# Performance work log

Hardware: AMD Instinct MI355X
Metric: run time of the kernel (lower is better)

## Reference

```python
import jax, jax.numpy as jnp
import numpy as np

B, L, D = 16384, 50, 32  # batch, history length, embedding_dim
NU, NI, NC = 100000, 100000, 1000


def setup_inputs() -> dict:
    key = jax.random.key(0)
    ks = jax.random.split(key, 16)
    customer_id = jax.random.randint(ks[0], (B,), 0, NU)
    candidate_good = jax.random.randint(ks[1], (B,), 0, NI)
    candidate_class = jax.random.randint(ks[2], (B,), 0, NC)
    history_goods = jax.random.randint(ks[3], (B, L), 0, NI)
    history_classes = jax.random.randint(ks[4], (B, L), 0, NC)
    user_table = jax.random.normal(ks[5], (NU, D), jnp.float32) * 0.05
    item_table = jax.random.normal(ks[6], (NI, D), jnp.float32) * 0.05
    item_table = item_table.at[0].set(0.0)  # padding_idx=0
    cat_table = jax.random.normal(ks[7], (NC, D), jnp.float32) * 0.05
    cat_table = cat_table.at[0].set(0.0)  # padding_idx=0
    # attention net: Linear(4*2D=256 -> 80), Linear(80 -> 1)
    aw1 = jax.random.normal(ks[8], (4 * 2 * D, 80), jnp.float32) * 0.05
    ab1 = jnp.zeros((80,), jnp.float32)
    aw2 = jax.random.normal(ks[9], (80, 1), jnp.float32) * 0.05
    ab2 = jnp.zeros((1,), jnp.float32)
    # final mlp: 5D=160 -> 256 -> 128 -> 1
    mw1 = jax.random.normal(ks[10], (5 * D, 256), jnp.float32) * 0.05
    mb1 = jnp.zeros((256,), jnp.float32)
    mw2 = jax.random.normal(ks[11], (256, 128), jnp.float32) * 0.05
    mb2 = jnp.zeros((128,), jnp.float32)
    mw3 = jax.random.normal(ks[12], (128, 1), jnp.float32) * 0.05
    mb3 = jnp.zeros((1,), jnp.float32)
    return dict(customer_id=customer_id, candidate_good=candidate_good,
                candidate_class=candidate_class, history_goods=history_goods,
                history_classes=history_classes, user_table=user_table,
                item_table=item_table, cat_table=cat_table,
                aw1=aw1, ab1=ab1, aw2=aw2, ab2=ab2,
                mw1=mw1, mb1=mb1, mw2=mw2, mb2=mb2, mw3=mw3, mb3=mb3)


def reference(customer_id, candidate_good, candidate_class, history_goods,
              history_classes, user_table, item_table, cat_table,
              aw1, ab1, aw2, ab2, mw1, mb1, mw2, mb2, mw3, mb3):
    user_emb = user_table[customer_id]                               # [B, D]
    cand = jnp.concatenate([item_table[candidate_good],
                            cat_table[candidate_class]], axis=-1)    # [B, 2D]
    hist = jnp.concatenate([item_table[history_goods],
                            cat_table[history_classes]], axis=-1)    # [B, L, 2D]
    q = jnp.broadcast_to(cand[:, None, :], hist.shape)               # [B, L, 2D]
    info = jnp.concatenate([q, hist, q - hist, q * hist], axis=-1)   # [B, L, 8D]
    h = jax.nn.relu(info @ aw1 + ab1)                                # [B, L, 80]
    scores = (h @ aw2 + ab2)[..., 0]                                 # [B, L]
    mask = history_goods != 0
    scores = jnp.where(mask, scores, -1e9)
    weights = jax.nn.softmax(scores, axis=1)                         # [B, L]
    att = jnp.einsum('bl,bld->bd', weights, hist)                    # [B, 2D]
    combined = jnp.concatenate([user_emb, cand, att], axis=-1)       # [B, 5D]
    z = jax.nn.relu(combined @ mw1 + mb1)
    z = jax.nn.relu(z @ mw2 + mb2)
    out = (z @ mw3 + mb3)[..., 0]                                    # [B]
    return out
```

## Files before the change

### kernel.cpp

```cpp
#include <hip/hip_runtime.h>
#include <hip/hip_bf16.h>
#include <math.h>

#define LHIST 50

typedef __attribute__((ext_vector_type(8))) short bf16x8;
typedef __attribute__((ext_vector_type(8))) unsigned short u16x8;
typedef __attribute__((ext_vector_type(4))) unsigned u32x4;
typedef __attribute__((ext_vector_type(4))) float f32x4;

__device__ __forceinline__ unsigned short f2bf(float f) {
    union { float f; unsigned u; } v; v.f = f;
    unsigned r = v.u + 0x7fff + ((v.u >> 16) & 1);
    return (unsigned short)(r >> 16);
}
__device__ __forceinline__ float bf2f(unsigned short h) {
    return __builtin_bit_cast(float, (unsigned)h << 16);
}
__device__ __forceinline__ unsigned pk2(float lo, float hi) {
    __hip_bfloat162 h = __float22bfloat162_rn(make_float2(lo, hi));
    unsigned u;
    __builtin_memcpy(&u, &h, 4);
    return u;
}
__device__ __forceinline__ f32x4 mfma16(bf16x8 a, bf16x8 b, f32x4 c) {
    return __builtin_amdgcn_mfma_f32_16x16x32_bf16(a, b, c, 0, 0, 0);
}
__device__ __forceinline__ bf16x8 mulq(u16x8 h, float4 qa, float4 qb) {
    u32x4 r;
    r[0] = pk2(bf2f(h[0]) * qa.x, bf2f(h[1]) * qa.y);
    r[1] = pk2(bf2f(h[2]) * qa.z, bf2f(h[3]) * qa.w);
    r[2] = pk2(bf2f(h[4]) * qb.x, bf2f(h[5]) * qb.y);
    r[3] = pk2(bf2f(h[6]) * qb.z, bf2f(h[7]) * qb.w);
    return __builtin_bit_cast(bf16x8, r);
}


__global__ void prep_kernel(const float* __restrict__ aw1,
                            const float* __restrict__ mw1,
                            const float* __restrict__ mw2,
                            const float* __restrict__ item_table,
                            const float* __restrict__ cat_table,
                            int itemN, int catN,
                            unsigned short* __restrict__ W13fb,
                            unsigned short* __restrict__ Bmfb,
                            unsigned short* __restrict__ W4fb,
                            unsigned short* __restrict__ W1f,
                            unsigned short* __restrict__ W2f,
                            unsigned short* __restrict__ itemb,
                            unsigned short* __restrict__ catb) {
    int i = blockIdx.x * 256 + threadIdx.x;
    int i8 = i * 8;
    if (i8 + 7 < itemN) {
        float4 a = *(const float4*)&item_table[i8];
        float4 b = *(const float4*)&item_table[i8 + 4];
        uint4 r;
        r.x = pk2(a.x, a.y); r.y = pk2(a.z, a.w);
        r.z = pk2(b.x, b.y); r.w = pk2(b.z, b.w);
        *(uint4*)&itemb[i8] = r;
    }
    if (i8 + 7 < catN) {
        float4 a = *(const float4*)&cat_table[i8];
        float4 b = *(const float4*)&cat_table[i8 + 4];
        uint4 r;
        r.x = pk2(a.x, a.y); r.y = pk2(a.z, a.w);
        r.z = pk2(b.x, b.y); r.w = pk2(b.z, b.w);
        *(uint4*)&catb[i8] = r;
    }
    if (i < 5120) {
        int kk = i / 80, n = i - kk * 80;
        int nt = n >> 4, colw = n & 15, ks = kk >> 5, r = kk & 31, qd = r >> 3, off = r & 7;
        int d = ((nt * 2 + ks) * 64 + qd * 16 + colw) * 8 + off;
        Bmfb[d]  = f2bf(aw1[(64 + kk) * 80 + n] - aw1[(128 + kk) * 80 + n]);
        W4fb[d]  = f2bf(aw1[(192 + kk) * 80 + n]);
        W13fb[d] = f2bf(aw1[kk * 80 + n] + aw1[(128 + kk) * 80 + n]);
    }
    if (i < 40960) {
        int kk = i >> 8, n = i & 255;
        int nt = n >> 4, colw = n & 15, ks = kk >> 5, r = kk & 31, qd = r >> 3, off = r & 7;
        W1f[((nt * 5 + ks) * 64 + qd * 16 + colw) * 8 + off] = f2bf(mw1[i]);
    }
    if (i < 32768) {
        int kk = i >> 7, n = i & 127;
        int nt = n >> 4, colw = n & 15, ks = kk >> 5, r = kk & 31, qd = r >> 3, off = r & 7;
        W2f[((nt * 8 + ks) * 64 + qd * 16 + colw) * 8 + off] = f2bf(mw2[i]);
    }
}


#define BIAS_JT(JT, OUT) { \
    bf16x8 w0 = *(const bf16x8*)&W13fb[((JT * 2 + 0) * 64 + lane) * 8]; \
    bf16x8 w1 = *(const bf16x8*)&W13fb[((JT * 2 + 1) * 64 + lane) * 8]; \
    f32x4 a = (f32x4){0.f, 0.f, 0.f, 0.f}; \
    a = mfma16(w0, qbi, a); \
    a = mfma16(w1, qbc, a); \
    float4 b4 = *(const float4*)&ab1[JT * 16 + quad * 4]; \
    a[0] += b4.x; a[1] += b4.y; a[2] += b4.z; a[3] += b4.w; \
    OUT = a; }

#define SCORE_JT(JT, ACCB, VIB, VCB, HQI, HQC, P) { \
    bf16x8 a23_0 = *(const bf16x8*)&Bmfb[((JT * 2 + 0) * 64 + lane) * 8]; \
    bf16x8 a23_1 = *(const bf16x8*)&Bmfb[((JT * 2 + 1) * 64 + lane) * 8]; \
    bf16x8 a4_0  = *(const bf16x8*)&W4fb[((JT * 2 + 0) * 64 + lane) * 8]; \
    bf16x8 a4_1  = *(const bf16x8*)&W4fb[((JT * 2 + 1) * 64 + lane) * 8]; \
    f32x4 acc = ACCB; \
    acc = mfma16(a23_0, VIB, acc); \
    acc = mfma16(a23_1, VCB, acc); \
    acc = mfma16(a4_0, HQI, acc); \
    acc = mfma16(a4_1, HQC, acc); \
    float4 a2 = *(const float4*)&aw2[JT * 16 + quad * 4]; \
    P += fmaxf(acc[0], 0.f) * a2.x + fmaxf(acc[1], 0.f) * a2.y \
       + fmaxf(acc[2], 0.f) * a2.z + fmaxf(acc[3], 0.f) * a2.w; }

#define SCORE_MI(VI, VC, HQI, HQC, PX) { \
    bf16x8 vib = __builtin_bit_cast(bf16x8, VI); \
    bf16x8 vcb = __builtin_bit_cast(bf16x8, VC); \
    float p = 0.f; \
    SCORE_JT(0, accb0, vib, vcb, HQI, HQC, p) \
    SCORE_JT(1, accb1, vib, vcb, HQI, HQC, p) \
    SCORE_JT(2, accb2, vib, vcb, HQI, HQC, p) \
    SCORE_JT(3, accb3, vib, vcb, HQI, HQC, p) \
    SCORE_JT(4, accb4, vib, vcb, HQI, HQC, p) \
    p += __shfl_xor(p, 16); \
    p += __shfl_xor(p, 32); \
    PX = p; }

#define ATT_ACC(VI, VC, W) { \
    ai0 += (W) * bf2f(VI[0]); ai1 += (W) * bf2f(VI[1]); \
    ai2 += (W) * bf2f(VI[2]); ai3 += (W) * bf2f(VI[3]); \
    ai4 += (W) * bf2f(VI[4]); ai5 += (W) * bf2f(VI[5]); \
    ai6 += (W) * bf2f(VI[6]); ai7 += (W) * bf2f(VI[7]); \
    ac0 += (W) * bf2f(VC[0]); ac1 += (W) * bf2f(VC[1]); \
    ac2 += (W) * bf2f(VC[2]); ac3 += (W) * bf2f(VC[3]); \
    ac4 += (W) * bf2f(VC[4]); ac5 += (W) * bf2f(VC[5]); \
    ac6 += (W) * bf2f(VC[6]); ac7 += (W) * bf2f(VC[7]); }

__global__ void __launch_bounds__(256, 3) attn_kernel(
    const int* __restrict__ cid, const int* __restrict__ cg,
    const int* __restrict__ cc,  const int* __restrict__ hg,
    const int* __restrict__ hc,
    const float* __restrict__ user_table, const float* __restrict__ item_table,
    const float* __restrict__ cat_table,
    const float* __restrict__ ab1, const float* __restrict__ aw2,
    const unsigned short* __restrict__ W13fb, const unsigned short* __restrict__ Bmfb,
    const unsigned short* __restrict__ W4fb,
    const unsigned short* __restrict__ itemb, const unsigned short* __restrict__ catb,
    float* __restrict__ combined)
{
    __shared__ float red[4][1056];
    __shared__ float sh_sc[2][64];
    __shared__ float sh_att[4][64];

    const int t = threadIdx.x;
    const int wv = t >> 6;
    const int lane = t & 63;
    const int quad = lane >> 4;
    const int col = lane & 15;
    const int bb = wv >> 1;
    const int hwv = wv & 1;
    const int hoff = hwv * 32;
    const int b = blockIdx.x * 2 + bb;

    const int cgb = cg[b], ccb = cc[b];

    const int hb = b * LHIST;
    int l1 = hoff + 16 + col;
    int l1c = (l1 < LHIST) ? l1 : 0;
    int ig0 = hg[hb + hoff + col], ic0 = hc[hb + hoff + col];
    int ig1 = hg[hb + l1c],        ic1 = hc[hb + l1c];
    bool bad0 = (ig0 == 0);
    bool bad1 = (l1 >= LHIST) || (ig1 == 0);

    u16x8 vi0 = *(const u16x8*)&itemb[(size_t)ig0 * 32 + quad * 8];
    u16x8 vi1 = *(const u16x8*)&itemb[(size_t)ig1 * 32 + quad * 8];
    u16x8 vc0 = *(const u16x8*)&catb[(size_t)ic0 * 32 + quad * 8];
    u16x8 vc1 = *(const u16x8*)&catb[(size_t)ic1 * 32 + quad * 8];

    const float4 qia = *(const float4*)&item_table[(size_t)cgb * 32 + quad * 8];
    const float4 qib = *(const float4*)&item_table[(size_t)cgb * 32 + quad * 8 + 4];
    const float4 qca = *(const float4*)&cat_table[(size_t)ccb * 32 + quad * 8];
    const float4 qcb = *(const float4*)&cat_table[(size_t)ccb * 32 + quad * 8 + 4];

    f32x4 accb0, accb1, accb2, accb3, accb4;
    {
        u32x4 u, v;
        u[0] = pk2(qia.x, qia.y); u[1] = pk2(qia.z, qia.w);
        u[2] = pk2(qib.x, qib.y); u[3] = pk2(qib.z, qib.w);
        v[0] = pk2(qca.x, qca.y); v[1] = pk2(qca.z, qca.w);
        v[2] = pk2(qcb.x, qcb.y); v[3] = pk2(qcb.z, qcb.w);
        bf16x8 qbi = __builtin_bit_cast(bf16x8, u);
        bf16x8 qbc = __builtin_bit_cast(bf16x8, v);
        BIAS_JT(0, accb0)
        BIAS_JT(1, accb1)
        BIAS_JT(2, accb2)
        BIAS_JT(3, accb3)
        BIAS_JT(4, accb4)
    }

    bf16x8 hqi0 = mulq(vi0, qia, qib);
    bf16x8 hqc0 = mulq(vc0, qca, qcb);
    bf16x8 hqi1 = mulq(vi1, qia, qib);
    bf16x8 hqc1 = mulq(vc1, qca, qcb);

    float px0, px1;
    SCORE_MI(vi0, vc0, hqi0, hqc0, px0)
    SCORE_MI(vi1, vc1, hqi1, hqc1, px1)

    if (quad == 0) {
        sh_sc[bb][hoff + col]      = bad0 ? -1e9f : px0;
        sh_sc[bb][hoff + 16 + col] = bad1 ? -1e9f : px1;
    }
    __syncthreads();

    float sc = (lane < LHIST) ? sh_sc[bb][lane] : -INFINITY;
    float m = sc;
    m = fmaxf(m, __shfl_xor(m, 32));
    m = fmaxf(m, __shfl_xor(m, 16));
    m = fmaxf(m, __shfl_xor(m, 8));
    m = fmaxf(m, __shfl_xor(m, 4));
    m = fmaxf(m, __shfl_xor(m, 2));
    m = fmaxf(m, __shfl_xor(m, 1));
    float e = (lane < LHIST) ? __expf(sc - m) : 0.f;
    float ssum = e;
    ssum += __shfl_xor(ssum, 32);
    ssum += __shfl_xor(ssum, 16);
    ssum += __shfl_xor(ssum, 8);
    ssum += __shfl_xor(ssum, 4);
    ssum += __shfl_xor(ssum, 2);
    ssum += __shfl_xor(ssum, 1);
    float w = e / ssum;

    float wl0 = __shfl(w, hoff + col);
    float wl1 = __shfl(w, hoff + 16 + col);

    float ai0 = 0.f, ai1 = 0.f, ai2 = 0.f, ai3 = 0.f;
    float ai4 = 0.f, ai5 = 0.f, ai6 = 0.f, ai7 = 0.f;
    float ac0 = 0.f, ac1 = 0.f, ac2 = 0.f, ac3 = 0.f;
    float ac4 = 0.f, ac5 = 0.f, ac6 = 0.f, ac7 = 0.f;
    ATT_ACC(vi0, vc0, wl0)
    ATT_ACC(vi1, vc1, wl1)

    float* myrow = &red[wv][col * 66];
    *(float2*)&myrow[quad * 8 + 0] = make_float2(ai0, ai1);
    *(float2*)&myrow[quad * 8 + 2] = make_float2(ai2, ai3);
    *(float2*)&myrow[quad * 8 + 4] = make_float2(ai4, ai5);
    *(float2*)&myrow[quad * 8 + 6] = make_float2(ai6, ai7);
    *(float2*)&myrow[33 + quad * 8 + 0] = make_float2(ac0, ac1);
    *(float2*)&myrow[33 + quad * 8 + 2] = make_float2(ac2, ac3);
    *(float2*)&myrow[33 + quad * 8 + 4] = make_float2(ac4, ac5);
    *(float2*)&myrow[33 + quad * 8 + 6] = make_float2(ac6, ac7);
    int colIdx = (lane < 32) ? lane : 33 + (lane - 32);
    float s = 0.f;
    #pragma unroll
    for (int c = 0; c < 16; ++c) s += red[wv][c * 66 + colIdx];
    sh_att[wv][lane] = s;
    __syncthreads();

    if (hwv == 0) {
        float* crow = combined + (size_t)b * 160;
        const int cidb = cid[b];
        crow[lane] = (lane < 32) ? user_table[(size_t)cidb * 32 + lane]
                                 : item_table[(size_t)cgb * 32 + (lane - 32)];
        if (lane < 32) crow[64 + lane] = cat_table[(size_t)ccb * 32 + lane];
        crow[96 + lane] = sh_att[bb * 2][lane] + sh_att[bb * 2 + 1][lane];
    }
}

__global__ void __launch_bounds__(256, 4) mlp_kernel(
    const float* __restrict__ combined,
    const unsigned short* __restrict__ W1f, const unsigned short* __restrict__ W2f,
    const float* __restrict__ mb1, const float* __restrict__ mb2,
    const float* __restrict__ mw3, const float* __restrict__ mb3,
    float* __restrict__ out)
{
    __shared__ __align__(16) unsigned short shA1[5120];
    __shared__ __align__(16) unsigned short shA2[8192];
    __shared__ float sh_part[4][32];

    const int t = threadIdx.x;
    const int b0 = blockIdx.x * 32;
    const int wv = t >> 6;
    const int lane = t & 63;
    const int quad = lane >> 4;
    const int col = lane & 15;

    for (int i = t; i < 1280; i += 256) {
        int m = i / 40;
        int s = i - m * 40;
        int k0 = s * 4;
        float4 v = *(const float4*)&combined[(size_t)(b0 + m) * 160 + k0];
        int mt = m >> 4, colm = m & 15;
        int ks = k0 >> 5, qd = (k0 >> 3) & 3, off = k0 & 7;
        ushort4 r; r.x = f2bf(v.x); r.y = f2bf(v.y); r.z = f2bf(v.z); r.w = f2bf(v.w);
        *(ushort4*)&shA1[((mt * 5 + ks) * 64 + qd * 16 + colm) * 8 + off] = r;
    }
    __syncthreads();

    f32x4 acc1[2][4];
    #pragma unroll
    for (int mt = 0; mt < 2; ++mt)
        #pragma unroll
        for (int j = 0; j < 4; ++j) acc1[mt][j] = (f32x4){0.f, 0.f, 0.f, 0.f};
    #pragma unroll
    for (int ks = 0; ks < 5; ++ks) {
        bf16x8 a0 = *(const bf16x8*)&shA1[(ks * 64 + lane) * 8];
        bf16x8 a1 = *(const bf16x8*)&shA1[((5 + ks) * 64 + lane) * 8];
        #pragma unroll
        for (int j = 0; j < 4; ++j) {
            int ntg = wv * 4 + j;
            bf16x8 bw = *(const bf16x8*)&W1f[((ntg * 5 + ks) * 64 + lane) * 8];
            acc1[0][j] = __builtin_amdgcn_mfma_f32_16x16x32_bf16(a0, bw, acc1[0][j], 0, 0, 0);
            acc1[1][j] = __builtin_amdgcn_mfma_f32_16x16x32_bf16(a1, bw, acc1[1][j], 0, 0, 0);
        }
    }
    #pragma unroll
    for (int j = 0; j < 4; ++j) {
        int n = (wv * 4 + j) * 16 + col;
        float bj = mb1[n];
        int ks2 = n >> 5, qd2 = (n >> 3) & 3, off2 = n & 7;
        #pragma unroll
        for (int mt = 0; mt < 2; ++mt)
            #pragma unroll
            for (int i = 0; i < 4; ++i) {
                float z = fmaxf(acc1[mt][j][i] + bj, 0.f);
                shA2[((mt * 8 + ks2) * 64 + qd2 * 16 + quad * 4 + i) * 8 + off2] = f2bf(z);
            }
    }
    __syncthreads();

    f32x4 acc2[2][2];
    #pragma unroll
    for (int mt = 0; mt < 2; ++mt)
        #pragma unroll
        for (int jj = 0; jj < 2; ++jj) acc2[mt][jj] = (f32x4){0.f, 0.f, 0.f, 0.f};
    #pragma unroll
    for (int ks = 0; ks < 8; ++ks) {
        bf16x8 a0 = *(const bf16x8*)&shA2[(ks * 64 + lane) * 8];
        bf16x8 a1 = *(const bf16x8*)&shA2[((8 + ks) * 64 + lane) * 8];
        #pragma unroll
        for (int jj = 0; jj < 2; ++jj) {
            int ntg = wv * 2 + jj;
            bf16x8 bw = *(const bf16x8*)&W2f[((ntg * 8 + ks) * 64 + lane) * 8];
            acc2[0][jj] = __builtin_amdgcn_mfma_f32_16x16x32_bf16(a0, bw, acc2[0][jj], 0, 0, 0);
            acc2[1][jj] = __builtin_amdgcn_mfma_f32_16x16x32_bf16(a1, bw, acc2[1][jj], 0, 0, 0);
        }
    }
    #pragma unroll
    for (int mt = 0; mt < 2; ++mt) {
        #pragma unroll
        for (int i = 0; i < 4; ++i) {
            float p = 0.f;
            #pragma unroll
            for (int jj = 0; jj < 2; ++jj) {
                int n = (wv * 2 + jj) * 16 + col;
                float z = fmaxf(acc2[mt][jj][i] + mb2[n], 0.f);
                p += z * mw3[n];
            }
            p += __shfl_xor(p, 1);
            p += __shfl_xor(p, 2);
            p += __shfl_xor(p, 4);
            p += __shfl_xor(p, 8);
            if (col == 0) sh_part[wv][mt * 16 + quad * 4 + i] = p;
        }
    }
    __syncthreads();
    if (t < 32)
        out[b0 + t] = sh_part[0][t] + sh_part[1][t] + sh_part[2][t] + sh_part[3][t] + mb3[0];
}

extern "C" void kernel_launch(void* const* d_in, const int* in_sizes, int n_in,
                              void* d_out, int out_size, void* d_ws, size_t ws_size,
                              hipStream_t stream) {
    const int*   cid = (const int*)d_in[0];
    const int*   cg  = (const int*)d_in[1];
    const int*   cc  = (const int*)d_in[2];
    const int*   hg  = (const int*)d_in[3];
    const int*   hc  = (const int*)d_in[4];
    const float* user_table = (const float*)d_in[5];
    const float* item_table = (const float*)d_in[6];
    const float* cat_table  = (const float*)d_in[7];
    const float* aw1 = (const float*)d_in[8];
    const float* ab1 = (const float*)d_in[9];
    const float* aw2 = (const float*)d_in[10];
    const float* mw1 = (const float*)d_in[12];
    const float* mb1 = (const float*)d_in[13];
    const float* mw2 = (const float*)d_in[14];
    const float* mb2 = (const float*)d_in[15];
    const float* mw3 = (const float*)d_in[16];
    const float* mb3 = (const float*)d_in[17];
    float* out = (float*)d_out;

    const int B = in_sizes[0];
    const int itemN = in_sizes[6];
    const int catN  = in_sizes[7];
    float* ws = (float*)d_ws;
    unsigned short* W13fb = (unsigned short*)ws;
    unsigned short* Bmfb = (unsigned short*)(ws + 5120);
    unsigned short* W4fb = (unsigned short*)(ws + 7680);
    unsigned short* W1f  = (unsigned short*)(ws + 10240);
    unsigned short* W2f  = (unsigned short*)(ws + 30720);
    unsigned short* itemb = (unsigned short*)(ws + 47104);
    unsigned short* catb  = itemb + itemN;
    float* combined = ws + 47104 + (itemN + catN + 1) / 2;

    int n8 = (itemN + 7) / 8;
    int prep_grid = (n8 + 255) / 256;
    if (prep_grid < 160) prep_grid = 160;
    prep_kernel<<<prep_grid, 256, 0, stream>>>(aw1, mw1, mw2, item_table, cat_table,
                                               itemN, catN, W13fb, Bmfb, W4fb, W1f, W2f,
                                               itemb, catb);
    attn_kernel<<<B / 2, 256, 0, stream>>>(cid, cg, cc, hg, hc,
                                           user_table, item_table, cat_table,
                                           ab1, aw2, W13fb, Bmfb, W4fb, itemb, catb, combined);
    mlp_kernel<<<B / 32, 256, 0, stream>>>(combined, W1f, W2f,
                                           mb1, mb2, mw3, mb3, out);
}
```

Before: 183.3 us.

## Process one batch row per block with one history tile per wave

The attention kernel now assigns one batch element per 256-thread block, so each of the four waves handles 16 history positions instead of two waves each handling 32 positions across two batch rows. This halves per-thread register state (one history tile, no precomputed bias accumulators), and the launch bound is raised to 4 waves per SIMD for more occupancy. In exchange, each wave now recomputes the candidate-bias MFMAs itself, the grid doubles to B blocks, and one of the four waves covers positions 48-63, so 14 of its 16 history slots are padding. The query product now uses bf16-rounded candidate values instead of fp32.

```diff
diff --git a/kernel.cpp b/kernel.cpp
--- a/kernel.cpp
+++ b/kernel.cpp
@@ -26,12 +26,12 @@
 __device__ __forceinline__ f32x4 mfma16(bf16x8 a, bf16x8 b, f32x4 c) {
     return __builtin_amdgcn_mfma_f32_16x16x32_bf16(a, b, c, 0, 0, 0);
 }
-__device__ __forceinline__ bf16x8 mulq(u16x8 h, float4 qa, float4 qb) {
+__device__ __forceinline__ bf16x8 mulqp(u16x8 h, u16x8 qp) {
     u32x4 r;
-    r[0] = pk2(bf2f(h[0]) * qa.x, bf2f(h[1]) * qa.y);
-    r[1] = pk2(bf2f(h[2]) * qa.z, bf2f(h[3]) * qa.w);
-    r[2] = pk2(bf2f(h[4]) * qb.x, bf2f(h[5]) * qb.y);
-    r[3] = pk2(bf2f(h[6]) * qb.z, bf2f(h[7]) * qb.w);
+    r[0] = pk2(bf2f(h[0]) * bf2f(qp[0]), bf2f(h[1]) * bf2f(qp[1]));
+    r[1] = pk2(bf2f(h[2]) * bf2f(qp[2]), bf2f(h[3]) * bf2f(qp[3]));
+    r[2] = pk2(bf2f(h[4]) * bf2f(qp[4]), bf2f(h[5]) * bf2f(qp[5]));
+    r[3] = pk2(bf2f(h[6]) * bf2f(qp[6]), bf2f(h[7]) * bf2f(qp[7]));
     return __builtin_bit_cast(bf16x8, r);
 }
 
@@ -88,54 +88,26 @@
 }
 
 
-#define BIAS_JT(JT, OUT) { \
+#define JT_STEP(JT) { \
     bf16x8 w0 = *(const bf16x8*)&W13fb[((JT * 2 + 0) * 64 + lane) * 8]; \
     bf16x8 w1 = *(const bf16x8*)&W13fb[((JT * 2 + 1) * 64 + lane) * 8]; \
-    f32x4 a = (f32x4){0.f, 0.f, 0.f, 0.f}; \
-    a = mfma16(w0, qbi, a); \
-    a = mfma16(w1, qbc, a); \
-    float4 b4 = *(const float4*)&ab1[JT * 16 + quad * 4]; \
-    a[0] += b4.x; a[1] += b4.y; a[2] += b4.z; a[3] += b4.w; \
-    OUT = a; }
-
-#define SCORE_JT(JT, ACCB, VIB, VCB, HQI, HQC, P) { \
+    f32x4 acc = (f32x4){0.f, 0.f, 0.f, 0.f}; \
+    acc = mfma16(w0, __builtin_bit_cast(bf16x8, qbi), acc); \
+    acc = mfma16(w1, __builtin_bit_cast(bf16x8, qbc), acc); \
     bf16x8 a23_0 = *(const bf16x8*)&Bmfb[((JT * 2 + 0) * 64 + lane) * 8]; \
     bf16x8 a23_1 = *(const bf16x8*)&Bmfb[((JT * 2 + 1) * 64 + lane) * 8]; \
-    bf16x8 a4_0  = *(const bf16x8*)&W4fb[((JT * 2 + 0) * 64 + lane) * 8]; \
-    bf16x8 a4_1  = *(const bf16x8*)&W4fb[((JT * 2 + 1) * 64 + lane) * 8]; \
-    f32x4 acc = ACCB; \
-    acc = mfma16(a23_0, VIB, acc); \
-    acc = mfma16(a23_1, VCB, acc); \
-    acc = mfma16(a4_0, HQI, acc); \
-    acc = mfma16(a4_1, HQC, acc); \
+    acc = mfma16(a23_0, __builtin_bit_cast(bf16x8, vi), acc); \
+    acc = mfma16(a23_1, __builtin_bit_cast(bf16x8, vc), acc); \
+    bf16x8 a4_0 = *(const bf16x8*)&W4fb[((JT * 2 + 0) * 64 + lane) * 8]; \
+    bf16x8 a4_1 = *(const bf16x8*)&W4fb[((JT * 2 + 1) * 64 + lane) * 8]; \
+    acc = mfma16(a4_0, hqi, acc); \
+    acc = mfma16(a4_1, hqc, acc); \
+    float4 b4 = *(const float4*)&ab1[JT * 16 + quad * 4]; \
     float4 a2 = *(const float4*)&aw2[JT * 16 + quad * 4]; \
-    P += fmaxf(acc[0], 0.f) * a2.x + fmaxf(acc[1], 0.f) * a2.y \
-       + fmaxf(acc[2], 0.f) * a2.z + fmaxf(acc[3], 0.f) * a2.w; }
-
-#define SCORE_MI(VI, VC, HQI, HQC, PX) { \
-    bf16x8 vib = __builtin_bit_cast(bf16x8, VI); \
-    bf16x8 vcb = __builtin_bit_cast(bf16x8, VC); \
-    float p = 0.f; \
-    SCORE_JT(0, accb0, vib, vcb, HQI, HQC, p) \
-    SCORE_JT(1, accb1, vib, vcb, HQI, HQC, p) \
-    SCORE_JT(2, accb2, vib, vcb, HQI, HQC, p) \
-    SCORE_JT(3, accb3, vib, vcb, HQI, HQC, p) \
-    SCORE_JT(4, accb4, vib, vcb, HQI, HQC, p) \
-    p += __shfl_xor(p, 16); \
-    p += __shfl_xor(p, 32); \
-    PX = p; }
-
-#define ATT_ACC(VI, VC, W) { \
-    ai0 += (W) * bf2f(VI[0]); ai1 += (W) * bf2f(VI[1]); \
-    ai2 += (W) * bf2f(VI[2]); ai3 += (W) * bf2f(VI[3]); \
-    ai4 += (W) * bf2f(VI[4]); ai5 += (W) * bf2f(VI[5]); \
-    ai6 += (W) * bf2f(VI[6]); ai7 += (W) * bf2f(VI[7]); \
-    ac0 += (W) * bf2f(VC[0]); ac1 += (W) * bf2f(VC[1]); \
-    ac2 += (W) * bf2f(VC[2]); ac3 += (W) * bf2f(VC[3]); \
-    ac4 += (W) * bf2f(VC[4]); ac5 += (W) * bf2f(VC[5]); \
-    ac6 += (W) * bf2f(VC[6]); ac7 += (W) * bf2f(VC[7]); }
-
-__global__ void __launch_bounds__(256, 3) attn_kernel(
+    p += fmaxf(acc[0] + b4.x, 0.f) * a2.x + fmaxf(acc[1] + b4.y, 0.f) * a2.y \
+       + fmaxf(acc[2] + b4.z, 0.f) * a2.z + fmaxf(acc[3] + b4.w, 0.f) * a2.w; }
+
+__global__ void __launch_bounds__(256, 4) attn_kernel(
     const int* __restrict__ cid, const int* __restrict__ cg,
     const int* __restrict__ cc,  const int* __restrict__ hg,
     const int* __restrict__ hc,
@@ -148,7 +120,7 @@
     float* __restrict__ combined)
 {
     __shared__ float red[4][1056];
-    __shared__ float sh_sc[2][64];
+    __shared__ float sh_sc[64];
     __shared__ float sh_att[4][64];
 
     const int t = threadIdx.x;
@@ -156,63 +128,51 @@
     const int lane = t & 63;
     const int quad = lane >> 4;
     const int col = lane & 15;
-    const int bb = wv >> 1;
-    const int hwv = wv & 1;
-    const int hoff = hwv * 32;
-    const int b = blockIdx.x * 2 + bb;
+    const int b = blockIdx.x;
 
     const int cgb = cg[b], ccb = cc[b];
 
     const int hb = b * LHIST;
-    int l1 = hoff + 16 + col;
-    int l1c = (l1 < LHIST) ? l1 : 0;
-    int ig0 = hg[hb + hoff + col], ic0 = hc[hb + hoff + col];
-    int ig1 = hg[hb + l1c],        ic1 = hc[hb + l1c];
-    bool bad0 = (ig0 == 0);
-    bool bad1 = (l1 >= LHIST) || (ig1 == 0);
-
-    u16x8 vi0 = *(const u16x8*)&itemb[(size_t)ig0 * 32 + quad * 8];
-    u16x8 vi1 = *(const u16x8*)&itemb[(size_t)ig1 * 32 + quad * 8];
-    u16x8 vc0 = *(const u16x8*)&catb[(size_t)ic0 * 32 + quad * 8];
-    u16x8 vc1 = *(const u16x8*)&catb[(size_t)ic1 * 32 + quad * 8];
-
-    const float4 qia = *(const float4*)&item_table[(size_t)cgb * 32 + quad * 8];
-    const float4 qib = *(const float4*)&item_table[(size_t)cgb * 32 + quad * 8 + 4];
-    const float4 qca = *(const float4*)&cat_table[(size_t)ccb * 32 + quad * 8];
-    const float4 qcb = *(const float4*)&cat_table[(size_t)ccb * 32 + quad * 8 + 4];
-
-    f32x4 accb0, accb1, accb2, accb3, accb4;
+    int l = wv * 16 + col;
+    int lc = (l < LHIST) ? l : 0;
+    int ig = hg[hb + lc];
+    int ic = hc[hb + lc];
+    bool bad = (l >= LHIST) || (ig == 0);
+
+    u16x8 vi = *(const u16x8*)&itemb[(size_t)ig * 32 + quad * 8];
+    u16x8 vc = *(const u16x8*)&catb[(size_t)ic * 32 + quad * 8];
+
+    u16x8 qbi, qbc;
     {
+        const float4 qia = *(const float4*)&item_table[(size_t)cgb * 32 + quad * 8];
+        const float4 qib = *(const float4*)&item_table[(size_t)cgb * 32 + quad * 8 + 4];
+        const float4 qca = *(const float4*)&cat_table[(size_t)ccb * 32 + quad * 8];
+        const float4 qcb = *(const float4*)&cat_table[(size_t)ccb * 32 + quad * 8 + 4];
         u32x4 u, v;
         u[0] = pk2(qia.x, qia.y); u[1] = pk2(qia.z, qia.w);
         u[2] = pk2(qib.x, qib.y); u[3] = pk2(qib.z, qib.w);
         v[0] = pk2(qca.x, qca.y); v[1] = pk2(qca.z, qca.w);
         v[2] = pk2(qcb.x, qcb.y); v[3] = pk2(qcb.z, qcb.w);
-        bf16x8 qbi = __builtin_bit_cast(bf16x8, u);
-        bf16x8 qbc = __builtin_bit_cast(bf16x8, v);
-        BIAS_JT(0, accb0)
-        BIAS_JT(1, accb1)
-        BIAS_JT(2, accb2)
-        BIAS_JT(3, accb3)
-        BIAS_JT(4, accb4)
-    }
-
-    bf16x8 hqi0 = mulq(vi0, qia, qib);
-    bf16x8 hqc0 = mulq(vc0, qca, qcb);
-    bf16x8 hqi1 = mulq(vi1, qia, qib);
-    bf16x8 hqc1 = mulq(vc1, qca, qcb);
-
-    float px0, px1;
-    SCORE_MI(vi0, vc0, hqi0, hqc0, px0)
-    SCORE_MI(vi1, vc1, hqi1, hqc1, px1)
-
-    if (quad == 0) {
-        sh_sc[bb][hoff + col]      = bad0 ? -1e9f : px0;
-        sh_sc[bb][hoff + 16 + col] = bad1 ? -1e9f : px1;
-    }
-    __syncthreads();
-
-    float sc = (lane < LHIST) ? sh_sc[bb][lane] : -INFINITY;
+        qbi = __builtin_bit_cast(u16x8, u);
+        qbc = __builtin_bit_cast(u16x8, v);
+    }
+
+    bf16x8 hqi = mulqp(vi, qbi);
+    bf16x8 hqc = mulqp(vc, qbc);
+
+    float p = 0.f;
+    JT_STEP(0)
+    JT_STEP(1)
+    JT_STEP(2)
+    JT_STEP(3)
+    JT_STEP(4)
+    p += __shfl_xor(p, 16);
+    p += __shfl_xor(p, 32);
+
+    if (quad == 0) sh_sc[wv * 16 + col] = bad ? -1e9f : p;
+    __syncthreads();
+
+    float sc = sh_sc[lane];
     float m = sc;
     m = fmaxf(m, __shfl_xor(m, 32));
     m = fmaxf(m, __shfl_xor(m, 16));
@@ -220,7 +180,7 @@
     m = fmaxf(m, __shfl_xor(m, 4));
     m = fmaxf(m, __shfl_xor(m, 2));
     m = fmaxf(m, __shfl_xor(m, 1));
-    float e = (lane < LHIST) ? __expf(sc - m) : 0.f;
+    float e = __expf(sc - m);
     float ssum = e;
     ssum += __shfl_xor(ssum, 32);
     ssum += __shfl_xor(ssum, 16);
@@ -230,25 +190,17 @@
     ssum += __shfl_xor(ssum, 1);
     float w = e / ssum;
 
-    float wl0 = __shfl(w, hoff + col);
-    float wl1 = __shfl(w, hoff + 16 + col);
-
-    float ai0 = 0.f, ai1 = 0.f, ai2 = 0.f, ai3 = 0.f;
-    float ai4 = 0.f, ai5 = 0.f, ai6 = 0.f, ai7 = 0.f;
-    float ac0 = 0.f, ac1 = 0.f, ac2 = 0.f, ac3 = 0.f;
-    float ac4 = 0.f, ac5 = 0.f, ac6 = 0.f, ac7 = 0.f;
-    ATT_ACC(vi0, vc0, wl0)
-    ATT_ACC(vi1, vc1, wl1)
+    float wl = __shfl(w, wv * 16 + col);
 
     float* myrow = &red[wv][col * 66];
-    *(float2*)&myrow[quad * 8 + 0] = make_float2(ai0, ai1);
-    *(float2*)&myrow[quad * 8 + 2] = make_float2(ai2, ai3);
-    *(float2*)&myrow[quad * 8 + 4] = make_float2(ai4, ai5);
-    *(float2*)&myrow[quad * 8 + 6] = make_float2(ai6, ai7);
-    *(float2*)&myrow[33 + quad * 8 + 0] = make_float2(ac0, ac1);
-    *(float2*)&myrow[33 + quad * 8 + 2] = make_float2(ac2, ac3);
-    *(float2*)&myrow[33 + quad * 8 + 4] = make_float2(ac4, ac5);
-    *(float2*)&myrow[33 + quad * 8 + 6] = make_float2(ac6, ac7);
+    *(float2*)&myrow[quad * 8 + 0] = make_float2(wl * bf2f(vi[0]), wl * bf2f(vi[1]));
+    *(float2*)&myrow[quad * 8 + 2] = make_float2(wl * bf2f(vi[2]), wl * bf2f(vi[3]));
+    *(float2*)&myrow[quad * 8 + 4] = make_float2(wl * bf2f(vi[4]), wl * bf2f(vi[5]));
+    *(float2*)&myrow[quad * 8 + 6] = make_float2(wl * bf2f(vi[6]), wl * bf2f(vi[7]));
+    *(float2*)&myrow[33 + quad * 8 + 0] = make_float2(wl * bf2f(vc[0]), wl * bf2f(vc[1]));
+    *(float2*)&myrow[33 + quad * 8 + 2] = make_float2(wl * bf2f(vc[2]), wl * bf2f(vc[3]));
+    *(float2*)&myrow[33 + quad * 8 + 4] = make_float2(wl * bf2f(vc[4]), wl * bf2f(vc[5]));
+    *(float2*)&myrow[33 + quad * 8 + 6] = make_float2(wl * bf2f(vc[6]), wl * bf2f(vc[7]));
     int colIdx = (lane < 32) ? lane : 33 + (lane - 32);
     float s = 0.f;
     #pragma unroll
@@ -256,13 +208,16 @@
     sh_att[wv][lane] = s;
     __syncthreads();
 
-    if (hwv == 0) {
-        float* crow = combined + (size_t)b * 160;
+    float* crow = combined + (size_t)b * 160;
+    if (wv == 0) {
         const int cidb = cid[b];
         crow[lane] = (lane < 32) ? user_table[(size_t)cidb * 32 + lane]
                                  : item_table[(size_t)cgb * 32 + (lane - 32)];
+    } else if (wv == 1) {
         if (lane < 32) crow[64 + lane] = cat_table[(size_t)ccb * 32 + lane];
-        crow[96 + lane] = sh_att[bb * 2][lane] + sh_att[bb * 2 + 1][lane];
+    } else if (wv == 2) {
+        crow[96 + lane] = sh_att[0][lane] + sh_att[1][lane]
+                        + sh_att[2][lane] + sh_att[3][lane];
     }
 }
 
@@ -409,9 +364,9 @@
     prep_kernel<<<prep_grid, 256, 0, stream>>>(aw1, mw1, mw2, item_table, cat_table,
                                                itemN, catN, W13fb, Bmfb, W4fb, W1f, W2f,
                                                itemb, catb);
-    attn_kernel<<<B / 2, 256, 0, stream>>>(cid, cg, cc, hg, hc,
-                                           user_table, item_table, cat_table,
-                                           ab1, aw2, W13fb, Bmfb, W4fb, itemb, catb, combined);
+    attn_kernel<<<B, 256, 0, stream>>>(cid, cg, cc, hg, hc,
+                                       user_table, item_table, cat_table,
+                                       ab1, aw2, W13fb, Bmfb, W4fb, itemb, catb, combined);
     mlp_kernel<<<B / 32, 256, 0, stream>>>(combined, W1f, W2f,
                                            mb1, mb2, mw3, mb3, out);
 }
```

Result: slower. 229.7 us (+25.3%).

## Fuse final MLP into attention kernel, dropping the combined-feature buffer

Applied to the files above, without the earlier changes.

The attention kernel now writes each block's two combined feature rows straight into an LDS tile laid out for MFMA (zero-padded to 16 rows) and runs the 160→256→128→1 MLP itself. This removes the separate MLP launch and the global write and reread of the combined buffer. The cost is that each block's MLP uses only 2 of 16 rows of every MFMA tile, so 8x more MFMA work and weight reads per sample. LDS use per block also grows.

```diff
diff --git a/kernel.cpp b/kernel.cpp
--- a/kernel.cpp
+++ b/kernel.cpp
@@ -135,7 +135,7 @@
     ac4 += (W) * bf2f(VC[4]); ac5 += (W) * bf2f(VC[5]); \
     ac6 += (W) * bf2f(VC[6]); ac7 += (W) * bf2f(VC[7]); }
 
-__global__ void __launch_bounds__(256, 3) attn_kernel(
+__global__ void __launch_bounds__(256, 3) fused_kernel(
     const int* __restrict__ cid, const int* __restrict__ cg,
     const int* __restrict__ cc,  const int* __restrict__ hg,
     const int* __restrict__ hc,
@@ -145,11 +145,17 @@
     const unsigned short* __restrict__ W13fb, const unsigned short* __restrict__ Bmfb,
     const unsigned short* __restrict__ W4fb,
     const unsigned short* __restrict__ itemb, const unsigned short* __restrict__ catb,
-    float* __restrict__ combined)
+    const unsigned short* __restrict__ W1f, const unsigned short* __restrict__ W2f,
+    const float* __restrict__ mb1, const float* __restrict__ mb2,
+    const float* __restrict__ mw3, const float* __restrict__ mb3,
+    float* __restrict__ out)
 {
-    __shared__ float red[4][1056];
+    __shared__ __align__(16) float red[4][1056];
     __shared__ float sh_sc[2][64];
     __shared__ float sh_att[4][64];
+    __shared__ __align__(16) unsigned short A1f[2560];
+    __shared__ __align__(16) unsigned short A2f[4096];
+    __shared__ float sh_part[4][4];
 
     const int t = threadIdx.x;
     const int wv = t >> 6;
@@ -162,6 +168,8 @@
     const int b = blockIdx.x * 2 + bb;
 
     const int cgb = cg[b], ccb = cc[b];
+
+    if (t < 160) ((uint4*)A1f)[t] = (uint4){0, 0, 0, 0};
 
     const int hb = b * LHIST;
     int l1 = hoff + 16 + col;
@@ -257,115 +265,72 @@
     __syncthreads();
 
     if (hwv == 0) {
-        float* crow = combined + (size_t)b * 160;
         const int cidb = cid[b];
-        crow[lane] = (lane < 32) ? user_table[(size_t)cidb * 32 + lane]
-                                 : item_table[(size_t)cgb * 32 + (lane - 32)];
-        if (lane < 32) crow[64 + lane] = cat_table[(size_t)ccb * 32 + lane];
-        crow[96 + lane] = sh_att[bb * 2][lane] + sh_att[bb * 2 + 1][lane];
-    }
-}
-
-__global__ void __launch_bounds__(256, 4) mlp_kernel(
-    const float* __restrict__ combined,
-    const unsigned short* __restrict__ W1f, const unsigned short* __restrict__ W2f,
-    const float* __restrict__ mb1, const float* __restrict__ mb2,
-    const float* __restrict__ mw3, const float* __restrict__ mb3,
-    float* __restrict__ out)
-{
-    __shared__ __align__(16) unsigned short shA1[5120];
-    __shared__ __align__(16) unsigned short shA2[8192];
-    __shared__ float sh_part[4][32];
-
-    const int t = threadIdx.x;
-    const int b0 = blockIdx.x * 32;
-    const int wv = t >> 6;
-    const int lane = t & 63;
-    const int quad = lane >> 4;
-    const int col = lane & 15;
-
-    for (int i = t; i < 1280; i += 256) {
-        int m = i / 40;
-        int s = i - m * 40;
-        int k0 = s * 4;
-        float4 v = *(const float4*)&combined[(size_t)(b0 + m) * 160 + k0];
-        int mt = m >> 4, colm = m & 15;
-        int ks = k0 >> 5, qd = (k0 >> 3) & 3, off = k0 & 7;
-        ushort4 r; r.x = f2bf(v.x); r.y = f2bf(v.y); r.z = f2bf(v.z); r.w = f2bf(v.w);
-        *(ushort4*)&shA1[((mt * 5 + ks) * 64 + qd * 16 + colm) * 8 + off] = r;
-    }
-    __syncthreads();
-
-    f32x4 acc1[2][4];
-    #pragma unroll
-    for (int mt = 0; mt < 2; ++mt)
-        #pragma unroll
-        for (int j = 0; j < 4; ++j) acc1[mt][j] = (f32x4){0.f, 0.f, 0.f, 0.f};
+        float v1 = (lane < 32) ? user_table[(size_t)cidb * 32 + lane]
+                               : item_table[(size_t)cgb * 32 + (lane - 32)];
+        int k = lane;
+        A1f[((k >> 5) * 64 + ((k >> 3) & 3) * 16 + bb) * 8 + (k & 7)] = f2bf(v1);
+        if (lane < 32) {
+            float v2 = cat_table[(size_t)ccb * 32 + lane];
+            k = 64 + lane;
+            A1f[((k >> 5) * 64 + ((k >> 3) & 3) * 16 + bb) * 8 + (k & 7)] = f2bf(v2);
+        }
+        float v3 = sh_att[bb * 2][lane] + sh_att[bb * 2 + 1][lane];
+        k = 96 + lane;
+        A1f[((k >> 5) * 64 + ((k >> 3) & 3) * 16 + bb) * 8 + (k & 7)] = f2bf(v3);
+    }
+    __syncthreads();
+
+    f32x4 acc1_0 = (f32x4){0.f,0.f,0.f,0.f};
+    f32x4 acc1_1 = (f32x4){0.f,0.f,0.f,0.f};
+    f32x4 acc1_2 = (f32x4){0.f,0.f,0.f,0.f};
+    f32x4 acc1_3 = (f32x4){0.f,0.f,0.f,0.f};
     #pragma unroll
     for (int ks = 0; ks < 5; ++ks) {
-        bf16x8 a0 = *(const bf16x8*)&shA1[(ks * 64 + lane) * 8];
-        bf16x8 a1 = *(const bf16x8*)&shA1[((5 + ks) * 64 + lane) * 8];
-        #pragma unroll
-        for (int j = 0; j < 4; ++j) {
-            int ntg = wv * 4 + j;
-            bf16x8 bw = *(const bf16x8*)&W1f[((ntg * 5 + ks) * 64 + lane) * 8];
-            acc1[0][j] = __builtin_amdgcn_mfma_f32_16x16x32_bf16(a0, bw, acc1[0][j], 0, 0, 0);
-            acc1[1][j] = __builtin_amdgcn_mfma_f32_16x16x32_bf16(a1, bw, acc1[1][j], 0, 0, 0);
-        }
+        bf16x8 a0 = *(const bf16x8*)&A1f[(ks * 64 + lane) * 8];
+        acc1_0 = mfma16(a0, *(const bf16x8*)&W1f[(((wv * 4 + 0) * 5 + ks) * 64 + lane) * 8], acc1_0);
+        acc1_1 = mfma16(a0, *(const bf16x8*)&W1f[(((wv * 4 + 1) * 5 + ks) * 64 + lane) * 8], acc1_1);
+        acc1_2 = mfma16(a0, *(const bf16x8*)&W1f[(((wv * 4 + 2) * 5 + ks) * 64 + lane) * 8], acc1_2);
+        acc1_3 = mfma16(a0, *(const bf16x8*)&W1f[(((wv * 4 + 3) * 5 + ks) * 64 + lane) * 8], acc1_3);
     }
     #pragma unroll
     for (int j = 0; j < 4; ++j) {
+        f32x4 aj = (j == 0) ? acc1_0 : (j == 1) ? acc1_1 : (j == 2) ? acc1_2 : acc1_3;
         int n = (wv * 4 + j) * 16 + col;
         float bj = mb1[n];
         int ks2 = n >> 5, qd2 = (n >> 3) & 3, off2 = n & 7;
         #pragma unroll
-        for (int mt = 0; mt < 2; ++mt)
-            #pragma unroll
-            for (int i = 0; i < 4; ++i) {
-                float z = fmaxf(acc1[mt][j][i] + bj, 0.f);
-                shA2[((mt * 8 + ks2) * 64 + qd2 * 16 + quad * 4 + i) * 8 + off2] = f2bf(z);
-            }
-    }
-    __syncthreads();
-
-    f32x4 acc2[2][2];
-    #pragma unroll
-    for (int mt = 0; mt < 2; ++mt)
-        #pragma unroll
-        for (int jj = 0; jj < 2; ++jj) acc2[mt][jj] = (f32x4){0.f, 0.f, 0.f, 0.f};
+        for (int i = 0; i < 4; ++i) {
+            float z = fmaxf(aj[i] + bj, 0.f);
+            A2f[(ks2 * 64 + qd2 * 16 + quad * 4 + i) * 8 + off2] = f2bf(z);
+        }
+    }
+    __syncthreads();
+
+    f32x4 acc2_0 = (f32x4){0.f,0.f,0.f,0.f};
+    f32x4 acc2_1 = (f32x4){0.f,0.f,0.f,0.f};
     #pragma unroll
     for (int ks = 0; ks < 8; ++ks) {
-        bf16x8 a0 = *(const bf16x8*)&shA2[(ks * 64 + lane) * 8];
-        bf16x8 a1 = *(const bf16x8*)&shA2[((8 + ks) * 64 + lane) * 8];
-        #pragma unroll
-        for (int jj = 0; jj < 2; ++jj) {
-            int ntg = wv * 2 + jj;
-            bf16x8 bw = *(const bf16x8*)&W2f[((ntg * 8 + ks) * 64 + lane) * 8];
-            acc2[0][jj] = __builtin_amdgcn_mfma_f32_16x16x32_bf16(a0, bw, acc2[0][jj], 0, 0, 0);
-            acc2[1][jj] = __builtin_amdgcn_mfma_f32_16x16x32_bf16(a1, bw, acc2[1][jj], 0, 0, 0);
-        }
-    }
-    #pragma unroll
-    for (int mt = 0; mt < 2; ++mt) {
-        #pragma unroll
-        for (int i = 0; i < 4; ++i) {
-            float p = 0.f;
-            #pragma unroll
-            for (int jj = 0; jj < 2; ++jj) {
-                int n = (wv * 2 + jj) * 16 + col;
-                float z = fmaxf(acc2[mt][jj][i] + mb2[n], 0.f);
-                p += z * mw3[n];
-            }
-            p += __shfl_xor(p, 1);
-            p += __shfl_xor(p, 2);
-            p += __shfl_xor(p, 4);
-            p += __shfl_xor(p, 8);
-            if (col == 0) sh_part[wv][mt * 16 + quad * 4 + i] = p;
-        }
-    }
-    __syncthreads();
-    if (t < 32)
-        out[b0 + t] = sh_part[0][t] + sh_part[1][t] + sh_part[2][t] + sh_part[3][t] + mb3[0];
+        bf16x8 a0 = *(const bf16x8*)&A2f[(ks * 64 + lane) * 8];
+        acc2_0 = mfma16(a0, *(const bf16x8*)&W2f[(((wv * 2 + 0) * 8 + ks) * 64 + lane) * 8], acc2_0);
+        acc2_1 = mfma16(a0, *(const bf16x8*)&W2f[(((wv * 2 + 1) * 8 + ks) * 64 + lane) * 8], acc2_1);
+    }
+    #pragma unroll
+    for (int i = 0; i < 2; ++i) {
+        int n0 = (wv * 2 + 0) * 16 + col;
+        int n1 = (wv * 2 + 1) * 16 + col;
+        float p = fmaxf(acc2_0[i] + mb2[n0], 0.f) * mw3[n0]
+                + fmaxf(acc2_1[i] + mb2[n1], 0.f) * mw3[n1];
+        p += __shfl_xor(p, 1);
+        p += __shfl_xor(p, 2);
+        p += __shfl_xor(p, 4);
+        p += __shfl_xor(p, 8);
+        if (lane == 0) sh_part[wv][i] = p;
+    }
+    __syncthreads();
+    if (t < 2)
+        out[blockIdx.x * 2 + t] = sh_part[0][t] + sh_part[1][t]
+                                + sh_part[2][t] + sh_part[3][t] + mb3[0];
 }
 
 extern "C" void kernel_launch(void* const* d_in, const int* in_sizes, int n_in,
@@ -401,7 +366,6 @@
     unsigned short* W2f  = (unsigned short*)(ws + 30720);
     unsigned short* itemb = (unsigned short*)(ws + 47104);
     unsigned short* catb  = itemb + itemN;
-    float* combined = ws + 47104 + (itemN + catN + 1) / 2;
 
     int n8 = (itemN + 7) / 8;
     int prep_grid = (n8 + 255) / 256;
@@ -409,9 +373,8 @@
     prep_kernel<<<prep_grid, 256, 0, stream>>>(aw1, mw1, mw2, item_table, cat_table,
                                                itemN, catN, W13fb, Bmfb, W4fb, W1f, W2f,
                                                itemb, catb);
-    attn_kernel<<<B / 2, 256, 0, stream>>>(cid, cg, cc, hg, hc,
-                                           user_table, item_table, cat_table,
-                                           ab1, aw2, W13fb, Bmfb, W4fb, itemb, catb, combined);
-    mlp_kernel<<<B / 32, 256, 0, stream>>>(combined, W1f, W2f,
-                                           mb1, mb2, mw3, mb3, out);
-}
+    fused_kernel<<<B / 2, 256, 0, stream>>>(cid, cg, cc, hg, hc,
+                                            user_table, item_table, cat_table,
+                                            ab1, aw2, W13fb, Bmfb, W4fb, itemb, catb,
+                                            W1f, W2f, mb1, mb2, mw3, mb3, out);
+}
```

New measurement: 230.3 us. 25.6% more time.
